# Performance work log

Measured on AMD Instinct MI355X. Metric: run time of the kernel, lower is better.

The kernel has to match this reference:

```python
import jax, jax.numpy as jnp
import numpy as np

MARGIN = 0.3
NUM_CLASSES = 32  # includes label 0, which the mask logic treats specially


def setup_inputs() -> dict:
    key = jax.random.key(0)
    k1, k2 = jax.random.split(key)
    n, d = 4096, 2048
    inputs = jax.random.normal(k1, (n, d), dtype=jnp.float32)
    targets = jax.random.randint(k2, (n,), 0, NUM_CLASSES, dtype=jnp.int64)
    return {"inputs": inputs, "targets": targets}


def reference(inputs, targets):
    # Pairwise euclidean distance matrix [n, n]
    sq = jnp.sum(inputs * inputs, axis=1)  # [n]
    dist2 = sq[:, None] + sq[None, :] - 2.0 * (inputs @ inputs.T)
    dist = jnp.sqrt(jnp.maximum(dist2, 1e-12))

    # Mask semantics from the torch code:
    #   mask == 1  : same label (hard-positive pool; includes diagonal)
    #   mask == 0  : different labels AND at least one of the pair has label 0
    #   mask == -1 : different labels, both nonzero (excluded from mining)
    ti, tj = targets[:, None], targets[None, :]
    same = ti == tj
    zero_neg = (~same) & ((ti == 0) | (tj == 0))

    neg_inf = jnp.asarray(-jnp.inf, dist.dtype)
    pos_inf = jnp.asarray(jnp.inf, dist.dtype)
    dist_ap = jnp.max(jnp.where(same, dist, neg_inf), axis=1)      # hardest positive per row
    row_min = jnp.min(jnp.where(zero_neg, dist, pos_inf), axis=1)  # hardest label-0 negative

    # Torch code checks row 0 only (mask[0]) for the presence of mask==0 entries;
    # if row 0 has none, ALL dist_an are set to 0. Reproduce faithfully.
    row0_has_zero = jnp.any(zero_neg[0])
    dist_an = jnp.where(row0_has_zero, row_min, jnp.zeros_like(row_min))

    # MarginRankingLoss with y = 1: mean(relu(-(dist_an - dist_ap) + margin))
    loss = jnp.mean(jax.nn.relu(dist_ap - dist_an + MARGIN))
    return loss
```

## Files before the change

kernel.cpp:

```cpp
#include <hip/hip_runtime.h>
#include <hip/hip_bf16.h>
#include <math.h>

#define N 4096
#define K 2048
#define NC 32
#define MARGIN 0.3f

#define BK 128
#define NITER (K / BK)
#define DIAG_BLOCKS 288
#define CROSS_BLOCKS 192
#define GRID (DIAG_BLOCKS + CROSS_BLOCKS)

typedef float f32x4 __attribute__((ext_vector_type(4)));
typedef __bf16 bf16x8 __attribute__((ext_vector_type(8)));

__device__ __forceinline__ void glds16(const void* g, void* l) {
  __builtin_amdgcn_global_load_lds(
      (const __attribute__((address_space(1))) void*)g,
      (__attribute__((address_space(3))) void*)l, 16, 0, 0);
}

__device__ __forceinline__ int imin(int a, int b) { return a < b ? a : b; }

__global__ __launch_bounds__(256) void hist_kernel(
    const int* __restrict__ tg, int* __restrict__ cnt, int* __restrict__ off,
    int* __restrict__ cursor, int* __restrict__ flag, int* __restrict__ done) {
  __shared__ int h[NC];
  int t = threadIdx.x;
  if (t < NC) h[t] = 0;
  __syncthreads();
  const int4* tg4 = (const int4*)tg;
  for (int i = t; i < N / 4; i += 256) {
    int4 v = tg4[i];
    atomicAdd(&h[v.x], 1); atomicAdd(&h[v.y], 1);
    atomicAdd(&h[v.z], 1); atomicAdd(&h[v.w], 1);
  }
  __syncthreads();
  if (t == 0) {
    int acc = 0;
    for (int c = 0; c < NC; c++) {
      cnt[c] = h[c];
      off[c] = acc;
      cursor[c] = acc;
      acc += h[c];
    }
    int t0 = tg[0];
    flag[0] = (t0 == 0) ? (N - h[0] > 0) : (h[0] > 0);
    done[0] = 0;
  }
}

__global__ __launch_bounds__(256) void convert_kernel(
    const float* __restrict__ X, const int* __restrict__ tg,
    __bf16* __restrict__ Xg, float* __restrict__ sqg,
    unsigned int* __restrict__ ap, unsigned int* __restrict__ an,
    int* __restrict__ cursor) {
  int row = blockIdx.x;
  int t = threadIdx.x;
  const float* xr = X + (size_t)row * K;

  float4 v0 = ((const float4*)xr)[t * 2 + 0];
  float4 v1 = ((const float4*)xr)[t * 2 + 1];

  float s = v0.x * v0.x + v0.y * v0.y + v0.z * v0.z + v0.w * v0.w +
            v1.x * v1.x + v1.y * v1.y + v1.z * v1.z + v1.w * v1.w;

  bf16x8 b;
  b[0] = (__bf16)v0.x; b[1] = (__bf16)v0.y; b[2] = (__bf16)v0.z; b[3] = (__bf16)v0.w;
  b[4] = (__bf16)v1.x; b[5] = (__bf16)v1.y; b[6] = (__bf16)v1.z; b[7] = (__bf16)v1.w;

  #pragma unroll
  for (int m = 32; m; m >>= 1) s += __shfl_xor(s, m);

  __shared__ float wred[4];
  __shared__ int spos;
  if ((t & 63) == 0) wred[t >> 6] = s;
  if (t == 0) spos = atomicAdd(&cursor[tg[row]], 1);
  __syncthreads();
  int pos = spos;

  ((bf16x8*)(Xg + (size_t)pos * K))[t] = b;
  if (t == 0) {
    sqg[pos] = wred[0] + wred[1] + wred[2] + wred[3];
    ap[pos] = 0u;
    an[pos] = 0x7f800000u;
  }
}

__global__ __launch_bounds__(256) void gemm_reduce_kernel(
    const __bf16* __restrict__ Xg, const float* __restrict__ sqg,
    const int* __restrict__ cnt, const int* __restrict__ off,
    unsigned int* __restrict__ ap, unsigned int* __restrict__ an,
    const int* __restrict__ flag, int* __restrict__ done,
    float* __restrict__ out) {
  __shared__ __align__(16) __bf16 sA[2][64 * BK];
  __shared__ __align__(16) __bf16 sB[2][64 * BK];
  __shared__ int s_islast;
  __shared__ float wred[4];

  int b = blockIdx.x;
  int t = threadIdx.x;

  bool active = true, diag = true;
  int i0g = 0, iend = 1, j0g = 0, jend = 1;
  if (b < DIAG_BLOCKS) {
    int c = b / 9, sub = b % 9;
    int sti = sub / 3, stj = sub % 3;
    int o = off[c], n = cnt[c];
    if (n == 0 || sti * 64 >= n || stj * 64 >= n) active = false;
    i0g = o + sti * 64; iend = o + n;
    j0g = o + stj * 64; jend = o + n;
  } else {
    int idx = b - DIAG_BLOCKS;
    int it = idx >> 6, jt = idx & 63;
    int n0 = cnt[0];
    int j0 = n0 + jt * 64;
    if (n0 == 0 || it * 64 >= n0 || j0 >= N) active = false;
    i0g = it * 64; iend = n0;
    j0g = j0; jend = N;
    diag = false;
  }

  if (active) {
    int w = t >> 6, l = t & 63;
    int wi = w >> 1, wj = w & 1;
    int quad = l >> 4, lr = l & 15;

    const char* gA[4]; const char* gB[4];
    int rr = t >> 4, cbl = t & 15;
    int cbg = cbl ^ rr;
    #pragma unroll
    for (int r = 0; r < 4; r++) {
      int row_l = r * 16 + rr;
      int ra = imin(i0g + row_l, iend - 1);
      int rb = imin(j0g + row_l, jend - 1);
      gA[r] = (const char*)(Xg + (size_t)ra * K) + cbg * 16;
      gB[r] = (const char*)(Xg + (size_t)rb * K) + cbg * 16;
    }

    int aoff[2][4], boff[2][4];
    #pragma unroll
    for (int ti = 0; ti < 2; ti++)
      #pragma unroll
      for (int kc = 0; kc < 4; kc++) {
        int cb = kc * 4 + quad;
        int sw = (cb ^ lr) * 16;
        aoff[ti][kc] = (wi * 32 + ti * 16 + lr) * 256 + sw;
        boff[ti][kc] = (wj * 32 + ti * 16 + lr) * 256 + sw;
      }

    f32x4 acc[2][2];
    acc[0][0] = (f32x4)0.f; acc[0][1] = (f32x4)0.f;
    acc[1][0] = (f32x4)0.f; acc[1][1] = (f32x4)0.f;

    auto stage = [&](int buf, int itk) {
      int koff = itk * (BK * 2);
      char* la = (char*)sA + buf * 16384 + t * 16;
      char* lb = (char*)sB + buf * 16384 + t * 16;
      #pragma unroll
      for (int r = 0; r < 4; r++) {
        glds16(gA[r] + koff, la + r * 4096);
        glds16(gB[r] + koff, lb + r * 4096);
      }
    };

    auto compute = [&](int buf) {
      const char* bufA = (const char*)sA + buf * 16384;
      const char* bufB = (const char*)sB + buf * 16384;
      #pragma unroll
      for (int kc = 0; kc < 4; kc++) {
        bf16x8 a0 = *(const bf16x8*)(bufA + aoff[0][kc]);
        bf16x8 a1 = *(const bf16x8*)(bufA + aoff[1][kc]);
        bf16x8 b0 = *(const bf16x8*)(bufB + boff[0][kc]);
        bf16x8 b1 = *(const bf16x8*)(bufB + boff[1][kc]);
        acc[0][0] = __builtin_amdgcn_mfma_f32_16x16x32_bf16(a0, b0, acc[0][0], 0, 0, 0);
        acc[0][1] = __builtin_amdgcn_mfma_f32_16x16x32_bf16(a0, b1, acc[0][1], 0, 0, 0);
        acc[1][0] = __builtin_amdgcn_mfma_f32_16x16x32_bf16(a1, b0, acc[1][0], 0, 0, 0);
        acc[1][1] = __builtin_amdgcn_mfma_f32_16x16x32_bf16(a1, b1, acc[1][1], 0, 0, 0);
      }
    };

    stage(0, 0);
    for (int itk = 0; itk < NITER - 1; ++itk) {
      int cur = itk & 1;
      __builtin_amdgcn_s_barrier();
      stage(cur ^ 1, itk + 1);
      __builtin_amdgcn_s_waitcnt(0x0F78);
      __builtin_amdgcn_s_barrier();
      __builtin_amdgcn_sched_barrier(0);
      compute(cur);
    }
    __builtin_amdgcn_s_barrier();
    __builtin_amdgcn_s_waitcnt(0x0F70);
    __builtin_amdgcn_s_barrier();
    __builtin_amdgcn_sched_barrier(0);
    compute((NITER - 1) & 1);

    int jgc[2]; float sqj[2];
    #pragma unroll
    for (int tj = 0; tj < 2; tj++) {
      int jg = j0g + wj * 32 + tj * 16 + lr;
      jgc[tj] = imin(jg, jend - 1);
      sqj[tj] = sqg[jgc[tj]];
    }

    if (diag) {
      #pragma unroll
      for (int ti = 0; ti < 2; ti++) {
        #pragma unroll
        for (int r = 0; r < 4; r++) {
          int ig = i0g + wi * 32 + ti * 16 + quad * 4 + r;
          int igc = imin(ig, iend - 1);
          float sqi = sqg[igc];
          float apm = 0.f;
          #pragma unroll
          for (int tj = 0; tj < 2; tj++) {
            float d2 = sqi + sqj[tj] - 2.f * acc[ti][tj][r];
            apm = fmaxf(apm, sqrtf(fmaxf(d2, 1e-12f)));
          }
          #pragma unroll
          for (int m = 1; m < 16; m <<= 1) apm = fmaxf(apm, __shfl_xor(apm, m));
          if (lr == 0) atomicMax(ap + igc, __float_as_uint(apm));
        }
      }
    } else {
      float colmin[2] = {INFINITY, INFINITY};
      #pragma unroll
      for (int ti = 0; ti < 2; ti++) {
        #pragma unroll
        for (int r = 0; r < 4; r++) {
          int ig = i0g + wi * 32 + ti * 16 + quad * 4 + r;
          int igc = imin(ig, iend - 1);
          float sqi = sqg[igc];
          float anm = INFINITY;
          #pragma unroll
          for (int tj = 0; tj < 2; tj++) {
            float d2 = sqi + sqj[tj] - 2.f * acc[ti][tj][r];
            float d = sqrtf(fmaxf(d2, 1e-12f));
            anm = fminf(anm, d);
            colmin[tj] = fminf(colmin[tj], d);
          }
          #pragma unroll
          for (int m = 1; m < 16; m <<= 1) anm = fminf(anm, __shfl_xor(anm, m));
          if (lr == 0) atomicMin(an + igc, __float_as_uint(anm));
        }
      }
      #pragma unroll
      for (int tj = 0; tj < 2; tj++) {
        float v = colmin[tj];
        v = fminf(v, __shfl_xor(v, 16));
        v = fminf(v, __shfl_xor(v, 32));
        if (quad == 0) atomicMin(an + jgc[tj], __float_as_uint(v));
      }
    }
  }

  __syncthreads();
  if (t == 0) {
    __threadfence();
    int ticket = __hip_atomic_fetch_add(done, 1, __ATOMIC_ACQ_REL,
                                        __HIP_MEMORY_SCOPE_AGENT);
    s_islast = (ticket == GRID - 1);
  }
  __syncthreads();
  if (s_islast) {
    int has = flag[0];
    float s = 0.f;
    for (int i = t; i < N; i += 256) {
      unsigned int au = __hip_atomic_load(ap + i, __ATOMIC_RELAXED,
                                          __HIP_MEMORY_SCOPE_AGENT);
      unsigned int nu = __hip_atomic_load(an + i, __ATOMIC_RELAXED,
                                          __HIP_MEMORY_SCOPE_AGENT);
      float a = __uint_as_float(au);
      float bb = has ? __uint_as_float(nu) : 0.f;
      s += fmaxf(a - bb + MARGIN, 0.f);
    }
    #pragma unroll
    for (int m = 32; m; m >>= 1) s += __shfl_xor(s, m);
    if ((t & 63) == 0) wred[t >> 6] = s;
    __syncthreads();
    if (t == 0) out[0] = (wred[0] + wred[1] + wred[2] + wred[3]) / (float)N;
  }
}

extern "C" void kernel_launch(void* const* d_in, const int* in_sizes, int n_in,
                              void* d_out, int out_size, void* d_ws,
                              size_t ws_size, hipStream_t stream) {
  const float* X = (const float*)d_in[0];
  const int* tg = (const int*)d_in[1];
  float* out = (float*)d_out;

  char* ws = (char*)d_ws;
  __bf16* Xg = (__bf16*)ws;
  size_t o = (size_t)N * K * 2;
  float* sqg = (float*)(ws + o); o += (size_t)N * 4;
  unsigned int* ap = (unsigned int*)(ws + o); o += (size_t)N * 4;
  unsigned int* an = (unsigned int*)(ws + o); o += (size_t)N * 4;
  int* cnt = (int*)(ws + o); o += NC * 4;
  int* off = (int*)(ws + o); o += NC * 4;
  int* cur = (int*)(ws + o); o += NC * 4;
  int* flag = (int*)(ws + o); o += 4;
  int* done = (int*)(ws + o); o += 4;

  hist_kernel<<<1, 256, 0, stream>>>(tg, cnt, off, cur, flag, done);
  convert_kernel<<<N, 256, 0, stream>>>(X, tg, Xg, sqg, ap, an, cur);
  gemm_reduce_kernel<<<GRID, 256, 0, stream>>>(Xg, sqg, cnt, off, ap, an,
                                               flag, done, out);
}
```

Measured before the change: 141.9 us.

## Build a tile list and compute only upper-triangle tiles with symmetric reductions

A planning kernel now builds an explicit list of tiles. Diagonal class blocks cover only their upper triangle, and symmetric off-diagonal tiles feed both row and column max reductions, so roughly half of the same-class GEMM work is skipped. A persistent grid of 512 blocks loops over the list instead of launching a fixed block count that included many inactive blocks. The K-tile shrinks to 64 with a three-stage LDS pipeline and launch bounds allowing three blocks per unit, and sqrt is deferred until after the reduction. In exchange there is a serial tile-generation step and more atomics per tile.

```diff
diff --git a/kernel.cpp b/kernel.cpp
--- a/kernel.cpp
+++ b/kernel.cpp
@@ -7,11 +7,10 @@
 #define NC 32
 #define MARGIN 0.3f
 
-#define BK 128
+#define BK 64
 #define NITER (K / BK)
-#define DIAG_BLOCKS 288
-#define CROSS_BLOCKS 192
-#define GRID (DIAG_BLOCKS + CROSS_BLOCKS)
+#define GRID 512
+#define MAXTILES 4096
 
 typedef float f32x4 __attribute__((ext_vector_type(4)));
 typedef __bf16 bf16x8 __attribute__((ext_vector_type(8)));
@@ -24,10 +23,11 @@
 
 __device__ __forceinline__ int imin(int a, int b) { return a < b ? a : b; }
 
-__global__ __launch_bounds__(256) void hist_kernel(
-    const int* __restrict__ tg, int* __restrict__ cnt, int* __restrict__ off,
-    int* __restrict__ cursor, int* __restrict__ flag, int* __restrict__ done) {
-  __shared__ int h[NC];
+__global__ __launch_bounds__(256) void plan_kernel(
+    const int* __restrict__ tg, int* __restrict__ cursor,
+    int* __restrict__ flag, int* __restrict__ done, int* __restrict__ Tp,
+    int4* __restrict__ tiles) {
+  __shared__ int h[NC], soff[NC], stb[NC + 1];
   int t = threadIdx.x;
   if (t < NC) h[t] = 0;
   __syncthreads();
@@ -39,16 +39,43 @@
   }
   __syncthreads();
   if (t == 0) {
-    int acc = 0;
+    int acc = 0, tacc = 0;
     for (int c = 0; c < NC; c++) {
-      cnt[c] = h[c];
-      off[c] = acc;
+      int n = h[c];
+      soff[c] = acc;
       cursor[c] = acc;
-      acc += h[c];
-    }
-    int t0 = tg[0];
-    flag[0] = (t0 == 0) ? (N - h[0] > 0) : (h[0] > 0);
+      acc += n;
+      stb[c] = tacc;
+      int tt = (n + 63) >> 6;
+      tacc += (tt * (tt + 1)) >> 1;
+    }
+    stb[NC] = tacc;
+    int n0 = h[0], nz = N - n0;
+    int t0b = (n0 + 63) >> 6, tzb = (nz + 63) >> 6;
+    Tp[0] = tacc + ((n0 > 0 && nz > 0) ? t0b * tzb : 0);
+    flag[0] = (tg[0] == 0) ? (nz > 0) : (n0 > 0);
     done[0] = 0;
+  }
+  __syncthreads();
+  if (t < NC && h[t] > 0) {
+    int n = h[t], o = soff[t];
+    int tt = (n + 63) >> 6;
+    int idx = stb[t];
+    for (int si = 0; si < tt; si++)
+      for (int sj = si; sj < tt; sj++) {
+        int fl = (si < sj) ? 3 : 1;
+        tiles[idx++] = make_int4((o + si * 64) | (fl << 28), o + sj * 64,
+                                 o + n, o + n);
+      }
+  }
+  int n0 = h[0], nz = N - n0;
+  if (n0 > 0 && nz > 0) {
+    int t0b = (n0 + 63) >> 6, tzb = (nz + 63) >> 6;
+    int base = stb[NC];
+    for (int k2 = t; k2 < t0b * tzb; k2 += 256) {
+      int si = k2 / tzb, sj = k2 - si * tzb;
+      tiles[base + k2] = make_int4((si * 64) | (2 << 28), n0 + sj * 64, n0, N);
+    }
   }
 }
 
@@ -89,172 +116,151 @@
   }
 }
 
-__global__ __launch_bounds__(256) void gemm_reduce_kernel(
-    const __bf16* __restrict__ Xg, const float* __restrict__ sqg,
-    const int* __restrict__ cnt, const int* __restrict__ off,
+__global__ __launch_bounds__(256, 3) void gemm_reduce_kernel(
+    const __bf16* __restrict__ Xg, const float* __restrict__ sq,
+    const int* __restrict__ Tp, const int4* __restrict__ tiles,
+    const int* __restrict__ flag, int* __restrict__ done,
     unsigned int* __restrict__ ap, unsigned int* __restrict__ an,
-    const int* __restrict__ flag, int* __restrict__ done,
     float* __restrict__ out) {
-  __shared__ __align__(16) __bf16 sA[2][64 * BK];
-  __shared__ __align__(16) __bf16 sB[2][64 * BK];
+  __shared__ __align__(16) char sAB[3][16384];
   __shared__ int s_islast;
   __shared__ float wred[4];
 
-  int b = blockIdx.x;
   int t = threadIdx.x;
-
-  bool active = true, diag = true;
-  int i0g = 0, iend = 1, j0g = 0, jend = 1;
-  if (b < DIAG_BLOCKS) {
-    int c = b / 9, sub = b % 9;
-    int sti = sub / 3, stj = sub % 3;
-    int o = off[c], n = cnt[c];
-    if (n == 0 || sti * 64 >= n || stj * 64 >= n) active = false;
-    i0g = o + sti * 64; iend = o + n;
-    j0g = o + stj * 64; jend = o + n;
-  } else {
-    int idx = b - DIAG_BLOCKS;
-    int it = idx >> 6, jt = idx & 63;
-    int n0 = cnt[0];
-    int j0 = n0 + jt * 64;
-    if (n0 == 0 || it * 64 >= n0 || j0 >= N) active = false;
-    i0g = it * 64; iend = n0;
-    j0g = j0; jend = N;
-    diag = false;
-  }
-
-  if (active) {
-    int w = t >> 6, l = t & 63;
-    int wi = w >> 1, wj = w & 1;
-    int quad = l >> 4, lr = l & 15;
-
-    const char* gA[4]; const char* gB[4];
-    int rr = t >> 4, cbl = t & 15;
-    int cbg = cbl ^ rr;
-    #pragma unroll
-    for (int r = 0; r < 4; r++) {
-      int row_l = r * 16 + rr;
-      int ra = imin(i0g + row_l, iend - 1);
-      int rb = imin(j0g + row_l, jend - 1);
-      gA[r] = (const char*)(Xg + (size_t)ra * K) + cbg * 16;
-      gB[r] = (const char*)(Xg + (size_t)rb * K) + cbg * 16;
-    }
-
-    int aoff[2][4], boff[2][4];
-    #pragma unroll
-    for (int ti = 0; ti < 2; ti++)
-      #pragma unroll
-      for (int kc = 0; kc < 4; kc++) {
-        int cb = kc * 4 + quad;
-        int sw = (cb ^ lr) * 16;
-        aoff[ti][kc] = (wi * 32 + ti * 16 + lr) * 256 + sw;
-        boff[ti][kc] = (wj * 32 + ti * 16 + lr) * 256 + sw;
-      }
+  int w = t >> 6, l = t & 63;
+  int wi = w >> 1, wj = w & 1;
+  int quad = l >> 4, lr = l & 15;
+
+  int aoff[2][2], boff[2][2];
+  #pragma unroll
+  for (int ti2 = 0; ti2 < 2; ti2++)
+    #pragma unroll
+    for (int h = 0; h < 2; h++) {
+      int sw = (((h << 2) + quad) ^ (lr & 7)) << 4;
+      aoff[ti2][h] = (wi * 32 + ti2 * 16 + lr) * 128 + sw;
+      boff[ti2][h] = (wj * 32 + ti2 * 16 + lr) * 128 + sw + 8192;
+    }
+
+  int rr = t >> 3, slot = t & 7;
+  int T = Tp[0];
+
+  for (int tid = blockIdx.x; tid < T; tid += GRID) {
+    int4 dsc = tiles[tid];
+    unsigned fl = (unsigned)dsc.x >> 28;
+    int i0 = dsc.x & 0x0FFFFFFF;
+    int j0 = dsc.y, iend = dsc.z, jend = dsc.w;
+    bool diag = fl & 1, colside = (fl & 2) != 0;
+
+    const char* gA[2]; const char* gB[2];
+    #pragma unroll
+    for (int r = 0; r < 2; r++) {
+      int row_l = r * 32 + rr;
+      int cbg = slot ^ (row_l & 7);
+      int ia = imin(i0 + row_l, iend - 1);
+      int ja = imin(j0 + row_l, jend - 1);
+      gA[r] = (const char*)(Xg + (size_t)ia * K) + cbg * 16;
+      gB[r] = (const char*)(Xg + (size_t)ja * K) + cbg * 16;
+    }
 
     f32x4 acc[2][2];
     acc[0][0] = (f32x4)0.f; acc[0][1] = (f32x4)0.f;
     acc[1][0] = (f32x4)0.f; acc[1][1] = (f32x4)0.f;
 
-    auto stage = [&](int buf, int itk) {
-      int koff = itk * (BK * 2);
-      char* la = (char*)sA + buf * 16384 + t * 16;
-      char* lb = (char*)sB + buf * 16384 + t * 16;
+    auto stage = [&](int buf, int it) {
+      char* base = sAB[buf] + t * 16;
+      int koff = it * 128;
+      glds16(gA[0] + koff, base);
+      glds16(gA[1] + koff, base + 4096);
+      glds16(gB[0] + koff, base + 8192);
+      glds16(gB[1] + koff, base + 12288);
+    };
+
+    auto compute = [&](int buf) {
+      const char* base = sAB[buf];
+      bf16x8 af[2][2], bfr[2][2];
+      #pragma unroll
+      for (int ti2 = 0; ti2 < 2; ti2++)
+        #pragma unroll
+        for (int h = 0; h < 2; h++) {
+          af[ti2][h] = *(const bf16x8*)(base + aoff[ti2][h]);
+          bfr[ti2][h] = *(const bf16x8*)(base + boff[ti2][h]);
+        }
+      #pragma unroll
+      for (int h = 0; h < 2; h++)
+        #pragma unroll
+        for (int ti2 = 0; ti2 < 2; ti2++)
+          #pragma unroll
+          for (int tj2 = 0; tj2 < 2; tj2++)
+            acc[ti2][tj2] = __builtin_amdgcn_mfma_f32_16x16x32_bf16(
+                af[ti2][h], bfr[tj2][h], acc[ti2][tj2], 0, 0, 0);
+    };
+
+    stage(0, 0);
+    stage(1, 1);
+    int pbuf = 2, cbuf = 0;
+    for (int it = 0; it < NITER; ++it) {
+      if (it < NITER - 1) __builtin_amdgcn_s_waitcnt(0x0F74);
+      else __builtin_amdgcn_s_waitcnt(0x0F70);
+      __builtin_amdgcn_s_barrier();
+      if (it + 2 < NITER) {
+        stage(pbuf, it + 2);
+        pbuf = (pbuf == 2) ? 0 : pbuf + 1;
+      }
+      __builtin_amdgcn_sched_barrier(0);
+      compute(cbuf);
+      cbuf = (cbuf == 2) ? 0 : cbuf + 1;
+    }
+
+    int jgc[2]; float sqj[2];
+    #pragma unroll
+    for (int tj2 = 0; tj2 < 2; tj2++) {
+      jgc[tj2] = imin(j0 + wj * 32 + tj2 * 16 + lr, jend - 1);
+      sqj[tj2] = sq[jgc[tj2]];
+    }
+    float cred[2];
+    cred[0] = cred[1] = diag ? 0.f : INFINITY;
+
+    #pragma unroll
+    for (int ti2 = 0; ti2 < 2; ti2++) {
       #pragma unroll
       for (int r = 0; r < 4; r++) {
-        glds16(gA[r] + koff, la + r * 4096);
-        glds16(gB[r] + koff, lb + r * 4096);
+        int ir = imin(i0 + wi * 32 + ti2 * 16 + quad * 4 + r, iend - 1);
+        float sqi = sq[ir];
+        float v = diag ? 0.f : INFINITY;
+        #pragma unroll
+        for (int tj2 = 0; tj2 < 2; tj2++) {
+          float d2 = fmaxf(sqi + sqj[tj2] - 2.f * acc[ti2][tj2][r], 1e-12f);
+          v = diag ? fmaxf(v, d2) : fminf(v, d2);
+          cred[tj2] = diag ? fmaxf(cred[tj2], d2) : fminf(cred[tj2], d2);
+        }
+        #pragma unroll
+        for (int m = 1; m < 16; m <<= 1) {
+          float o = __shfl_xor(v, m);
+          v = diag ? fmaxf(v, o) : fminf(v, o);
+        }
+        if (lr == 0) {
+          unsigned int u = __float_as_uint(sqrtf(v));
+          if (diag) atomicMax(ap + ir, u);
+          else      atomicMin(an + ir, u);
+        }
       }
-    };
-
-    auto compute = [&](int buf) {
-      const char* bufA = (const char*)sA + buf * 16384;
-      const char* bufB = (const char*)sB + buf * 16384;
+    }
+    if (colside) {
       #pragma unroll
-      for (int kc = 0; kc < 4; kc++) {
-        bf16x8 a0 = *(const bf16x8*)(bufA + aoff[0][kc]);
-        bf16x8 a1 = *(const bf16x8*)(bufA + aoff[1][kc]);
-        bf16x8 b0 = *(const bf16x8*)(bufB + boff[0][kc]);
-        bf16x8 b1 = *(const bf16x8*)(bufB + boff[1][kc]);
-        acc[0][0] = __builtin_amdgcn_mfma_f32_16x16x32_bf16(a0, b0, acc[0][0], 0, 0, 0);
-        acc[0][1] = __builtin_amdgcn_mfma_f32_16x16x32_bf16(a0, b1, acc[0][1], 0, 0, 0);
-        acc[1][0] = __builtin_amdgcn_mfma_f32_16x16x32_bf16(a1, b0, acc[1][0], 0, 0, 0);
-        acc[1][1] = __builtin_amdgcn_mfma_f32_16x16x32_bf16(a1, b1, acc[1][1], 0, 0, 0);
+      for (int tj2 = 0; tj2 < 2; tj2++) {
+        float v = cred[tj2];
+        float o = __shfl_xor(v, 16);
+        v = diag ? fmaxf(v, o) : fminf(v, o);
+        o = __shfl_xor(v, 32);
+        v = diag ? fmaxf(v, o) : fminf(v, o);
+        if (quad == 0) {
+          unsigned int u = __float_as_uint(sqrtf(v));
+          if (diag) atomicMax(ap + jgc[tj2], u);
+          else      atomicMin(an + jgc[tj2], u);
+        }
       }
-    };
-
-    stage(0, 0);
-    for (int itk = 0; itk < NITER - 1; ++itk) {
-      int cur = itk & 1;
-      __builtin_amdgcn_s_barrier();
-      stage(cur ^ 1, itk + 1);
-      __builtin_amdgcn_s_waitcnt(0x0F78);
-      __builtin_amdgcn_s_barrier();
-      __builtin_amdgcn_sched_barrier(0);
-      compute(cur);
     }
     __builtin_amdgcn_s_barrier();
-    __builtin_amdgcn_s_waitcnt(0x0F70);
-    __builtin_amdgcn_s_barrier();
-    __builtin_amdgcn_sched_barrier(0);
-    compute((NITER - 1) & 1);
-
-    int jgc[2]; float sqj[2];
-    #pragma unroll
-    for (int tj = 0; tj < 2; tj++) {
-      int jg = j0g + wj * 32 + tj * 16 + lr;
-      jgc[tj] = imin(jg, jend - 1);
-      sqj[tj] = sqg[jgc[tj]];
-    }
-
-    if (diag) {
-      #pragma unroll
-      for (int ti = 0; ti < 2; ti++) {
-        #pragma unroll
-        for (int r = 0; r < 4; r++) {
-          int ig = i0g + wi * 32 + ti * 16 + quad * 4 + r;
-          int igc = imin(ig, iend - 1);
-          float sqi = sqg[igc];
-          float apm = 0.f;
-          #pragma unroll
-          for (int tj = 0; tj < 2; tj++) {
-            float d2 = sqi + sqj[tj] - 2.f * acc[ti][tj][r];
-            apm = fmaxf(apm, sqrtf(fmaxf(d2, 1e-12f)));
-          }
-          #pragma unroll
-          for (int m = 1; m < 16; m <<= 1) apm = fmaxf(apm, __shfl_xor(apm, m));
-          if (lr == 0) atomicMax(ap + igc, __float_as_uint(apm));
-        }
-      }
-    } else {
-      float colmin[2] = {INFINITY, INFINITY};
-      #pragma unroll
-      for (int ti = 0; ti < 2; ti++) {
-        #pragma unroll
-        for (int r = 0; r < 4; r++) {
-          int ig = i0g + wi * 32 + ti * 16 + quad * 4 + r;
-          int igc = imin(ig, iend - 1);
-          float sqi = sqg[igc];
-          float anm = INFINITY;
-          #pragma unroll
-          for (int tj = 0; tj < 2; tj++) {
-            float d2 = sqi + sqj[tj] - 2.f * acc[ti][tj][r];
-            float d = sqrtf(fmaxf(d2, 1e-12f));
-            anm = fminf(anm, d);
-            colmin[tj] = fminf(colmin[tj], d);
-          }
-          #pragma unroll
-          for (int m = 1; m < 16; m <<= 1) anm = fminf(anm, __shfl_xor(anm, m));
-          if (lr == 0) atomicMin(an + igc, __float_as_uint(anm));
-        }
-      }
-      #pragma unroll
-      for (int tj = 0; tj < 2; tj++) {
-        float v = colmin[tj];
-        v = fminf(v, __shfl_xor(v, 16));
-        v = fminf(v, __shfl_xor(v, 32));
-        if (quad == 0) atomicMin(an + jgc[tj], __float_as_uint(v));
-      }
-    }
   }
 
   __syncthreads();
@@ -295,17 +301,18 @@
   char* ws = (char*)d_ws;
   __bf16* Xg = (__bf16*)ws;
   size_t o = (size_t)N * K * 2;
-  float* sqg = (float*)(ws + o); o += (size_t)N * 4;
+  float* sq = (float*)(ws + o); o += (size_t)N * 4;
   unsigned int* ap = (unsigned int*)(ws + o); o += (size_t)N * 4;
   unsigned int* an = (unsigned int*)(ws + o); o += (size_t)N * 4;
-  int* cnt = (int*)(ws + o); o += NC * 4;
-  int* off = (int*)(ws + o); o += NC * 4;
-  int* cur = (int*)(ws + o); o += NC * 4;
+  int* cursor = (int*)(ws + o); o += NC * 4;
   int* flag = (int*)(ws + o); o += 4;
   int* done = (int*)(ws + o); o += 4;
-
-  hist_kernel<<<1, 256, 0, stream>>>(tg, cnt, off, cur, flag, done);
-  convert_kernel<<<N, 256, 0, stream>>>(X, tg, Xg, sqg, ap, an, cur);
-  gemm_reduce_kernel<<<GRID, 256, 0, stream>>>(Xg, sqg, cnt, off, ap, an,
-                                               flag, done, out);
-}
+  int* Tp = (int*)(ws + o); o += 4;
+  o = (o + 15) & ~(size_t)15;
+  int4* tiles = (int4*)(ws + o); o += (size_t)MAXTILES * 16;
+
+  plan_kernel<<<1, 256, 0, stream>>>(tg, cursor, flag, done, Tp, tiles);
+  convert_kernel<<<N, 256, 0, stream>>>(X, tg, Xg, sq, ap, an, cursor);
+  gemm_reduce_kernel<<<GRID, 256, 0, stream>>>(Xg, sq, Tp, tiles, flag, done,
+                                               ap, an, out);
+}
```

Measured after the change: 145.4 us. +2.4%, slower.
